# Kernel optimization log

Measured on AMD Instinct MI355X. Metric: run time of the kernel, lower is better.

## Reference

```python
import jax, jax.numpy as jnp
import numpy as np

# BinsCombinerLayer: the original keras layer implements, via two nested serial
# tf.scan loops, the quantity
#   out = (1 / num_bins) * sum_i dot(bin_output_i, centroids_i)
# i.e. the mean over bins of the expected value (probability-weighted centroid sum)
# of each bin. Here we vectorize it as a single einsum, batched over examples.

B, NUM_BINS, BIN_SIZE = 32768, 16, 128


def setup_inputs() -> dict:
    key = jax.random.key(0)
    k_in, k_c = jax.random.split(key)
    # per-example, per-bin class probabilities (e.g. softmax outputs)
    logits = jax.random.uniform(k_in, (B, NUM_BINS, BIN_SIZE), dtype=jnp.float32)
    inputs = logits / jnp.sum(logits, axis=-1, keepdims=True)  # normalized like probs
    # centroid value for each class of each bin (learned/fixed table)
    centroids = jax.random.normal(k_c, (NUM_BINS, BIN_SIZE), dtype=jnp.float32)
    return {"inputs": inputs, "centroids": centroids}


def reference(inputs, centroids):
    # expected value per bin: sum_j inputs[b, n, j] * centroids[n, j]
    # then averaged over bins (the original divides the bin-sum by num_bins)
    num_bins = inputs.shape[1]
    ev = jnp.einsum("bns,ns->b", inputs, centroids)  # [B]
    return ev / num_bins
```

## Files before the change

### kernel.cpp

```cpp
#include <hip/hip_runtime.h>


#define BLOCK 256
#define WAVES_PER_BLOCK (BLOCK / 64)
#define ROW_F4 512

__global__ __launch_bounds__(BLOCK) void bins_combiner_kernel(
    const float4* __restrict__ in,
    const float4* __restrict__ cent,
    float* __restrict__ out,
    int B) {
    __shared__ float4 c_lds[ROW_F4];

    for (int i = threadIdx.x; i < ROW_F4; i += BLOCK) {
        c_lds[i] = cent[i];
    }
    __syncthreads();

    const int wave = threadIdx.x >> 6;
    const int lane = threadIdx.x & 63;
    const int waves_total = gridDim.x * WAVES_PER_BLOCK;

    for (int row = blockIdx.x * WAVES_PER_BLOCK + wave; row < B;
         row += waves_total) {
        const float4* rp = in + (size_t)row * ROW_F4;

        float acc = 0.0f;
#pragma unroll
        for (int k = 0; k < 8; ++k) {
            const int idx = k * 64 + lane;
            const float4 a = rp[idx];
            const float4 c = c_lds[idx];
            acc += a.x * c.x + a.y * c.y + a.z * c.z + a.w * c.w;
        }

#pragma unroll
        for (int off = 32; off > 0; off >>= 1) {
            acc += __shfl_down(acc, off, 64);
        }
        if (lane == 0) {
            out[row] = acc * (1.0f / 16.0f);
        }
    }
}

extern "C" void kernel_launch(void* const* d_in, const int* in_sizes, int n_in,
                              void* d_out, int out_size, void* d_ws, size_t ws_size,
                              hipStream_t stream) {
    const float4* in = (const float4*)d_in[0];
    const float4* cent = (const float4*)d_in[1];
    float* out = (float*)d_out;

    const int B = out_size;
    const int rows_per_block = WAVES_PER_BLOCK;
    const int grid = (B + rows_per_block - 1) / rows_per_block;

    bins_combiner_kernel<<<grid, BLOCK, 0, stream>>>(in, cent, out, B);
}
```

Before: 351.0 us.

## Use persistent grid with register-held centroids and two-row nontemporal loads

Replaces one-row-per-wave launch with a fixed grid where each wave processes a contiguous chunk of rows, two at a time. Centroids move from LDS into registers, which removes the per-block shared memory fill and barrier. Input loads use nontemporal hints and twice as many loads are in flight per wave, aimed at better streaming bandwidth. Register pressure rises and occupancy may drop.

```diff
diff --git a/kernel.cpp b/kernel.cpp
--- a/kernel.cpp
+++ b/kernel.cpp
@@ -1,45 +1,68 @@
 #include <hip/hip_runtime.h>
 
+
+typedef float fv4 __attribute__((ext_vector_type(4)));
 
 #define BLOCK 256
 #define WAVES_PER_BLOCK (BLOCK / 64)
 #define ROW_F4 512
+#define GRID 2048
 
 __global__ __launch_bounds__(BLOCK) void bins_combiner_kernel(
-    const float4* __restrict__ in,
-    const float4* __restrict__ cent,
+    const fv4* __restrict__ in,
+    const fv4* __restrict__ cent,
     float* __restrict__ out,
     int B) {
-    __shared__ float4 c_lds[ROW_F4];
-
-    for (int i = threadIdx.x; i < ROW_F4; i += BLOCK) {
-        c_lds[i] = cent[i];
-    }
-    __syncthreads();
-
-    const int wave = threadIdx.x >> 6;
     const int lane = threadIdx.x & 63;
+    const int wave_id = blockIdx.x * WAVES_PER_BLOCK + (threadIdx.x >> 6);
     const int waves_total = gridDim.x * WAVES_PER_BLOCK;
 
-    for (int row = blockIdx.x * WAVES_PER_BLOCK + wave; row < B;
-         row += waves_total) {
-        const float4* rp = in + (size_t)row * ROW_F4;
+    fv4 c[8];
+#pragma unroll
+    for (int k = 0; k < 8; ++k) {
+        c[k] = cent[k * 64 + lane];
+    }
 
-        float acc = 0.0f;
+    const int rows_per_wave = (B + waves_total - 1) / waves_total;
+    const int row0 = wave_id * rows_per_wave;
+    const int row_end = (row0 + rows_per_wave < B) ? row0 + rows_per_wave : B;
+
+    for (int r = row0; r < row_end; r += 2) {
+        const bool has2 = (r + 1) < row_end;
+        const int r1 = has2 ? (r + 1) : r;
+        const fv4* rp0 = in + (size_t)r * ROW_F4;
+        const fv4* rp1 = in + (size_t)r1 * ROW_F4;
+
+        fv4 a0[8], a1[8];
 #pragma unroll
         for (int k = 0; k < 8; ++k) {
-            const int idx = k * 64 + lane;
-            const float4 a = rp[idx];
-            const float4 c = c_lds[idx];
-            acc += a.x * c.x + a.y * c.y + a.z * c.z + a.w * c.w;
+            a0[k] = __builtin_nontemporal_load(&rp0[k * 64 + lane]);
+        }
+#pragma unroll
+        for (int k = 0; k < 8; ++k) {
+            a1[k] = __builtin_nontemporal_load(&rp1[k * 64 + lane]);
+        }
+
+        float acc0 = 0.0f, acc1 = 0.0f;
+#pragma unroll
+        for (int k = 0; k < 8; ++k) {
+            acc0 += a0[k].x * c[k].x + a0[k].y * c[k].y +
+                    a0[k].z * c[k].z + a0[k].w * c[k].w;
+        }
+#pragma unroll
+        for (int k = 0; k < 8; ++k) {
+            acc1 += a1[k].x * c[k].x + a1[k].y * c[k].y +
+                    a1[k].z * c[k].z + a1[k].w * c[k].w;
         }
 
 #pragma unroll
         for (int off = 32; off > 0; off >>= 1) {
-            acc += __shfl_down(acc, off, 64);
+            acc0 += __shfl_down(acc0, off, 64);
+            acc1 += __shfl_down(acc1, off, 64);
         }
         if (lane == 0) {
-            out[row] = acc * (1.0f / 16.0f);
+            out[r] = acc0 * (1.0f / 16.0f);
+            if (has2) out[r + 1] = acc1 * (1.0f / 16.0f);
         }
     }
 }
@@ -47,13 +70,10 @@
 extern "C" void kernel_launch(void* const* d_in, const int* in_sizes, int n_in,
                               void* d_out, int out_size, void* d_ws, size_t ws_size,
                               hipStream_t stream) {
-    const float4* in = (const float4*)d_in[0];
-    const float4* cent = (const float4*)d_in[1];
+    const fv4* in = (const fv4*)d_in[0];
+    const fv4* cent = (const fv4*)d_in[1];
     float* out = (float*)d_out;
 
     const int B = out_size;
-    const int rows_per_block = WAVES_PER_BLOCK;
-    const int grid = (B + rows_per_block - 1) / rows_per_block;
-
-    bins_combiner_kernel<<<grid, BLOCK, 0, stream>>>(in, cent, out, B);
+    bins_combiner_kernel<<<GRID, BLOCK, 0, stream>>>(in, cent, out, B);
 }
```

After: 330.1 us. 6.0% less time.
